# Optimization experiments

Measured on AMD Instinct MI355X. Metric: run time of the kernel, lower is better.

## Reference

```python
import jax, jax.numpy as jnp
import numpy as np

N_NODES = 50000


def gcn_conv(x, row, col, W, b, n_nodes):
    # x: [N, Cin], row/col: [E+N] (self-loops already appended)
    x = x @ W  # [N, Cout]
    deg = jax.ops.segment_sum(jnp.ones(col.shape, x.dtype), col, num_segments=n_nodes)
    dinv = jnp.where(deg > 0, jax.lax.rsqrt(deg), 0.0)
    norm = dinv[row] * dinv[col]  # [E+N]
    msgs = x[row] * norm[:, None]  # gather + scale, [E+N, Cout]
    out = jax.ops.segment_sum(msgs, col, num_segments=n_nodes)
    return out + b


def setup_inputs() -> dict:
    key = jax.random.key(0)
    ks = jax.random.split(key, 5)
    n, e = N_NODES, 640000
    d_in, d_h, d_out = 128, 128, 64
    x = jax.random.normal(ks[0], (n, d_in), dtype=jnp.float32)
    edge_index = jax.random.randint(ks[1], (2, e), 0, n, dtype=jnp.int64)
    s1 = 1.0 / np.sqrt(d_in)
    s2 = 1.0 / np.sqrt(d_h)
    W1 = jax.random.normal(ks[2], (d_in, d_h), dtype=jnp.float32) * s1
    W2 = jax.random.normal(ks[3], (d_h, d_h), dtype=jnp.float32) * s2
    Wl = jax.random.normal(ks[4], (d_h, d_out), dtype=jnp.float32) * s2
    return {
        "x": x, "edge_index": edge_index,
        "W1": W1, "b1": jnp.zeros((d_h,), jnp.float32),
        "W2": W2, "b2": jnp.zeros((d_h,), jnp.float32),
        "Wl": Wl, "bl": jnp.zeros((d_out,), jnp.float32),
    }


def reference(x, edge_index, W1, b1, W2, b2, Wl, bl):
    n = x.shape[0]
    loops = jnp.arange(n, dtype=edge_index.dtype)
    row = jnp.concatenate([edge_index[0], loops])  # add self-loops (PyG GCNConv)
    col = jnp.concatenate([edge_index[1], loops])
    h = jax.nn.relu(gcn_conv(x, row, col, W1, b1, n))  # dropout is identity in eval
    h = jax.nn.relu(gcn_conv(h, row, col, W2, b2, n))
    return h @ Wl + bl
```

## Files before the change

### kernel.cpp

```cpp
#include <hip/hip_runtime.h>

#define NN 50000
#define NE 640000
#define RB ((NN + 255) / 256)

struct __align__(8) edge_t { int r; float w; };

__global__ void k_detect(const unsigned* __restrict__ w, int* __restrict__ flag) {
    __shared__ int found;
    if (threadIdx.x == 0) found = 0;
    __syncthreads();
    int j = threadIdx.x * 2499;
    if (w[2 * j + 1] != 0u) atomicAdd(&found, 1);
    __syncthreads();
    if (threadIdx.x == 0) *flag = (found == 0) ? 1 : 0;
}

__device__ __forceinline__ int edge_at(const void* p, long long i, int m64) {
    if (m64) return (int)((const long long*)p)[i];
    return ((const int*)p)[i];
}

__global__ void k_count(const void* __restrict__ e, const int* __restrict__ flag,
                        int* __restrict__ deg) {
    int i = blockIdx.x * 256 + threadIdx.x;
    if (i >= NE) return;
    int m = *flag;
    int c = edge_at(e, (long long)NE + i, m);
    if ((unsigned)c < (unsigned)NN) atomicAdd(&deg[c], 1);
}

__global__ __launch_bounds__(256) void k_reduce(const int* __restrict__ deg,
                                                int* __restrict__ bsum) {
    __shared__ int s[256];
    int i = blockIdx.x * 256 + threadIdx.x;
    s[threadIdx.x] = (i < NN) ? deg[i] : 0;
    __syncthreads();
    for (int d = 128; d > 0; d >>= 1) {
        if (threadIdx.x < d) s[threadIdx.x] += s[threadIdx.x + d];
        __syncthreads();
    }
    if (threadIdx.x == 0) bsum[blockIdx.x] = s[0];
}

__global__ __launch_bounds__(256) void k_apply(const int* __restrict__ deg,
                                               const int* __restrict__ bsum,
                                               int* __restrict__ offs,
                                               int* __restrict__ cursor,
                                               float* __restrict__ dinv) {
    __shared__ int s[256];
    __shared__ int base_s;
    int t = threadIdx.x;
    int v = (t < RB && t < blockIdx.x) ? bsum[t] : 0;
    s[t] = v;
    __syncthreads();
    for (int d = 128; d > 0; d >>= 1) {
        if (t < d) s[t] += s[t + d];
        __syncthreads();
    }
    if (t == 0) base_s = s[0];
    __syncthreads();
    int base = base_s;
    __syncthreads();
    int i = blockIdx.x * 256 + t;
    int dg = (i < NN) ? deg[i] : 0;
    s[t] = dg;
    __syncthreads();
    for (int d = 1; d < 256; d <<= 1) {
        int u = (t >= d) ? s[t - d] : 0;
        __syncthreads();
        s[t] += u;
        __syncthreads();
    }
    if (i < NN) {
        int excl = base + s[t] - dg;
        offs[i] = excl;
        cursor[i] = excl;
        dinv[i] = rsqrtf((float)(dg + 1));
        if (i == NN - 1) offs[NN] = excl + dg;
    }
}

__global__ void k_scatter(const void* __restrict__ e, const int* __restrict__ flag,
                          int* __restrict__ cursor, edge_t* __restrict__ ew,
                          const float* __restrict__ dinv) {
    int i = blockIdx.x * 256 + threadIdx.x;
    if (i >= NE) return;
    int m = *flag;
    int c = edge_at(e, (long long)NE + i, m);
    if ((unsigned)c >= (unsigned)NN) return;
    int r = edge_at(e, (long long)i, m);
    r = min(max(r, 0), NN - 1);
    int p = atomicAdd(&cursor[c], 1);
    edge_t t2; t2.r = r; t2.w = dinv[r];
    ew[p] = t2;
}

__global__ __launch_bounds__(256) void k_gemm128(const float* __restrict__ A,
                                                 const float* __restrict__ W,
                                                 float* __restrict__ T) {
    __shared__ float Ws[64 * 128];
    int t = threadIdx.x;
    int rg = t >> 4, cg = t & 15;
    int row0 = blockIdx.x * 32 + rg * 2;
    const float4* a0 = (const float4*)(A + (long long)min(row0 + 0, NN - 1) * 128);
    const float4* a1 = (const float4*)(A + (long long)min(row0 + 1, NN - 1) * 128);
    float acc[2][8];
#pragma unroll
    for (int i = 0; i < 2; i++)
#pragma unroll
        for (int j = 0; j < 8; j++) acc[i][j] = 0.f;
#pragma unroll
    for (int h = 0; h < 2; h++) {
        __syncthreads();
#pragma unroll
        for (int i = 0; i < 8; i++)
            ((float4*)Ws)[t + 256 * i] = ((const float4*)(W + h * 64 * 128))[t + 256 * i];
        __syncthreads();
#pragma unroll 4
        for (int k4 = 0; k4 < 16; k4++) {
            float4 av0 = a0[h * 16 + k4];
            float4 av1 = a1[h * 16 + k4];
#pragma unroll
            for (int kk = 0; kk < 4; kk++) {
                float4 w0 = *(const float4*)&Ws[(k4 * 4 + kk) * 128 + cg * 4];
                float4 w1 = *(const float4*)&Ws[(k4 * 4 + kk) * 128 + cg * 4 + 64];
                float x0 = (kk == 0) ? av0.x : (kk == 1) ? av0.y : (kk == 2) ? av0.z : av0.w;
                float x1 = (kk == 0) ? av1.x : (kk == 1) ? av1.y : (kk == 2) ? av1.z : av1.w;
                acc[0][0] += x0 * w0.x; acc[0][1] += x0 * w0.y;
                acc[0][2] += x0 * w0.z; acc[0][3] += x0 * w0.w;
                acc[0][4] += x0 * w1.x; acc[0][5] += x0 * w1.y;
                acc[0][6] += x0 * w1.z; acc[0][7] += x0 * w1.w;
                acc[1][0] += x1 * w0.x; acc[1][1] += x1 * w0.y;
                acc[1][2] += x1 * w0.z; acc[1][3] += x1 * w0.w;
                acc[1][4] += x1 * w1.x; acc[1][5] += x1 * w1.y;
                acc[1][6] += x1 * w1.z; acc[1][7] += x1 * w1.w;
            }
        }
    }
#pragma unroll
    for (int i = 0; i < 2; i++) {
        int row = row0 + i;
        if (row < NN) {
            float4 v0 = {acc[i][0], acc[i][1], acc[i][2], acc[i][3]};
            float4 v1 = {acc[i][4], acc[i][5], acc[i][6], acc[i][7]};
            *(float4*)&T[(long long)row * 128 + cg * 4] = v0;
            *(float4*)&T[(long long)row * 128 + cg * 4 + 64] = v1;
        }
    }
}

__global__ __launch_bounds__(256) void k_gemm64(const float* __restrict__ A,
                                                const float* __restrict__ W,
                                                const float* __restrict__ b,
                                                float* __restrict__ T) {
    __shared__ float Ws[128 * 64];
    int t = threadIdx.x;
#pragma unroll
    for (int i = 0; i < 8; i++)
        ((float4*)Ws)[t + 256 * i] = ((const float4*)W)[t + 256 * i];
    __syncthreads();
    int rg = t >> 4, cg = t & 15;
    int row0 = blockIdx.x * 32 + rg * 2;
    const float4* a0 = (const float4*)(A + (long long)min(row0 + 0, NN - 1) * 128);
    const float4* a1 = (const float4*)(A + (long long)min(row0 + 1, NN - 1) * 128);
    float acc[2][4];
#pragma unroll
    for (int i = 0; i < 2; i++)
#pragma unroll
        for (int j = 0; j < 4; j++) acc[i][j] = 0.f;
#pragma unroll 4
    for (int k4 = 0; k4 < 32; k4++) {
        float4 av0 = a0[k4];
        float4 av1 = a1[k4];
#pragma unroll
        for (int kk = 0; kk < 4; kk++) {
            float4 w = *(const float4*)&Ws[(k4 * 4 + kk) * 64 + cg * 4];
            float x0 = (kk == 0) ? av0.x : (kk == 1) ? av0.y : (kk == 2) ? av0.z : av0.w;
            float x1 = (kk == 0) ? av1.x : (kk == 1) ? av1.y : (kk == 2) ? av1.z : av1.w;
            acc[0][0] += x0 * w.x; acc[0][1] += x0 * w.y;
            acc[0][2] += x0 * w.z; acc[0][3] += x0 * w.w;
            acc[1][0] += x1 * w.x; acc[1][1] += x1 * w.y;
            acc[1][2] += x1 * w.z; acc[1][3] += x1 * w.w;
        }
    }
    float4 bb = ((const float4*)b)[cg];
#pragma unroll
    for (int i = 0; i < 2; i++) {
        int row = row0 + i;
        if (row < NN) {
            float4 v = {acc[i][0] + bb.x, acc[i][1] + bb.y,
                        acc[i][2] + bb.z, acc[i][3] + bb.w};
            *(float4*)&T[(long long)row * 64 + cg * 4] = v;
        }
    }
}

__global__ __launch_bounds__(256) void k_agg(const float* __restrict__ X,
                                             const int* __restrict__ offs,
                                             const edge_t* __restrict__ ew,
                                             const float* __restrict__ dinv,
                                             const float* __restrict__ b,
                                             float* __restrict__ H) {
    int t = threadIdx.x;
    int node = blockIdx.x * 4 + (t >> 6);
    if (node >= NN) return;
    int lane = t & 63;
    int half = lane >> 5;
    int l32 = lane & 31;
    const float4* X4 = (const float4*)X;
    float dc = dinv[node];
    float4 acc = {0.f, 0.f, 0.f, 0.f};
    if (half == 0) {
        float4 s = X4[(long long)node * 32 + l32];
        acc.x = dc * s.x; acc.y = dc * s.y; acc.z = dc * s.z; acc.w = dc * s.w;
    }
    int e0 = offs[node], e1 = offs[node + 1];
    int n = e1 - e0;
    const edge_t* ep = ew + e0;
    int i = half;
    for (; i + 6 < n; i += 8) {
        edge_t m0 = ep[i], m1 = ep[i + 2], m2 = ep[i + 4], m3 = ep[i + 6];
        float4 v0 = X4[(long long)m0.r * 32 + l32];
        float4 v1 = X4[(long long)m1.r * 32 + l32];
        float4 v2 = X4[(long long)m2.r * 32 + l32];
        float4 v3 = X4[(long long)m3.r * 32 + l32];
        acc.x += m0.w * v0.x + m1.w * v1.x + m2.w * v2.x + m3.w * v3.x;
        acc.y += m0.w * v0.y + m1.w * v1.y + m2.w * v2.y + m3.w * v3.y;
        acc.z += m0.w * v0.z + m1.w * v1.z + m2.w * v2.z + m3.w * v3.z;
        acc.w += m0.w * v0.w + m1.w * v1.w + m2.w * v2.w + m3.w * v3.w;
    }
    for (; i < n; i += 2) {
        edge_t m = ep[i];
        float4 v = X4[(long long)m.r * 32 + l32];
        acc.x += m.w * v.x; acc.y += m.w * v.y;
        acc.z += m.w * v.z; acc.w += m.w * v.w;
    }
    float4 oth;
    oth.x = __shfl_xor(acc.x, 32);
    oth.y = __shfl_xor(acc.y, 32);
    oth.z = __shfl_xor(acc.z, 32);
    oth.w = __shfl_xor(acc.w, 32);
    float4 bb = ((const float4*)b)[l32];
    float4 o;
    o.x = fmaxf(dc * (acc.x + oth.x) + bb.x, 0.f);
    o.y = fmaxf(dc * (acc.y + oth.y) + bb.y, 0.f);
    o.z = fmaxf(dc * (acc.z + oth.z) + bb.z, 0.f);
    o.w = fmaxf(dc * (acc.w + oth.w) + bb.w, 0.f);
    if (half == 0)
        ((float4*)H)[(long long)node * 32 + l32] = o;
}

extern "C" void kernel_launch(void* const* d_in, const int* in_sizes, int n_in,
                              void* d_out, int out_size, void* d_ws, size_t ws_size,
                              hipStream_t stream) {
    const float* x  = (const float*)d_in[0];
    const void*  ei = d_in[1];
    const float* W1 = (const float*)d_in[2];
    const float* b1 = (const float*)d_in[3];
    const float* W2 = (const float*)d_in[4];
    const float* b2 = (const float*)d_in[5];
    const float* Wl = (const float*)d_in[6];
    const float* bl = (const float*)d_in[7];
    float* out = (float*)d_out;

    char* ws = (char*)d_ws;
    size_t off = 0;
    auto alloc = [&](size_t bytes) {
        void* p = ws + off;
        off += (bytes + 255) & ~(size_t)255;
        return p;
    };
    float*  t0     = (float*)alloc((size_t)NN * 128 * 4);
    float*  t1     = (float*)alloc((size_t)NN * 128 * 4);
    int*    deg    = (int*)alloc((size_t)NN * 4);
    int*    offs   = (int*)alloc((size_t)(NN + 1) * 4);
    int*    cursor = (int*)alloc((size_t)NN * 4);
    edge_t* ewbuf  = (edge_t*)alloc((size_t)NE * 8);
    float*  dinv   = (float*)alloc((size_t)NN * 4);
    int*    bsum   = (int*)alloc((size_t)RB * 4);
    int*    flag   = (int*)alloc(256);

    hipMemsetAsync(deg, 0, (size_t)NN * 4, stream);
    k_detect<<<1, 256, 0, stream>>>((const unsigned*)ei, flag);
    k_count<<<(NE + 255) / 256, 256, 0, stream>>>(ei, flag, deg);
    k_reduce<<<RB, 256, 0, stream>>>(deg, bsum);
    k_apply<<<RB, 256, 0, stream>>>(deg, bsum, offs, cursor, dinv);
    k_scatter<<<(NE + 255) / 256, 256, 0, stream>>>(ei, flag, cursor, ewbuf, dinv);

    int gb32 = (NN + 31) / 32;
    k_gemm128<<<gb32, 256, 0, stream>>>(x, W1, t0);
    k_agg<<<(NN + 3) / 4, 256, 0, stream>>>(t0, offs, ewbuf, dinv, b1, t1);
    k_gemm128<<<gb32, 256, 0, stream>>>(t1, W2, t0);
    k_agg<<<(NN + 3) / 4, 256, 0, stream>>>(t0, offs, ewbuf, dinv, b2, t1);
    k_gemm64<<<gb32, 256, 0, stream>>>(t1, Wl, bl, out);
}
```

Before: 329.5 us.

## Store transformed features in fp16 for aggregation and inline index-width detection

The GEMM outputs feeding the neighbor aggregation are now stored as fp16, and the aggregation kernel converts them back to fp32 after loading. This halves the bytes moved by the random-access gather, which dominates aggregation cost. Separately, the single-block width-detection kernel is removed and its check is folded into each block of the count and scatter kernels, saving a launch at the cost of a small redundant read per block. The fp16 storage adds rounding error to the hidden features relative to the fp32 reference.

New measurement: 308.0 us. 1.07x faster.

```diff
diff --git a/kernel.cpp b/kernel.cpp
--- a/kernel.cpp
+++ b/kernel.cpp
@@ -1,4 +1,5 @@
 #include <hip/hip_runtime.h>
+#include <hip/hip_fp16.h>
 
 #define NN 50000
 #define NE 640000
@@ -6,26 +7,25 @@
 
 struct __align__(8) edge_t { int r; float w; };
 
-__global__ void k_detect(const unsigned* __restrict__ w, int* __restrict__ flag) {
-    __shared__ int found;
-    if (threadIdx.x == 0) found = 0;
-    __syncthreads();
-    int j = threadIdx.x * 2499;
-    if (w[2 * j + 1] != 0u) atomicAdd(&found, 1);
-    __syncthreads();
-    if (threadIdx.x == 0) *flag = (found == 0) ? 1 : 0;
-}
-
 __device__ __forceinline__ int edge_at(const void* p, long long i, int m64) {
     if (m64) return (int)((const long long*)p)[i];
     return ((const int*)p)[i];
 }
 
-__global__ void k_count(const void* __restrict__ e, const int* __restrict__ flag,
-                        int* __restrict__ deg) {
+__device__ __forceinline__ int detect_m64(const unsigned* w, int tid) {
+    __shared__ int found;
+    if (tid == 0) found = 0;
+    __syncthreads();
+    if (tid < 256 && w[2 * tid + 1] != 0u) atomicAdd(&found, 1);
+    __syncthreads();
+    return (found == 0) ? 1 : 0;
+}
+
+__global__ __launch_bounds__(256) void k_count(const void* __restrict__ e,
+                                               int* __restrict__ deg) {
+    int m = detect_m64((const unsigned*)e, threadIdx.x);
     int i = blockIdx.x * 256 + threadIdx.x;
     if (i >= NE) return;
-    int m = *flag;
     int c = edge_at(e, (long long)NE + i, m);
     if ((unsigned)c < (unsigned)NN) atomicAdd(&deg[c], 1);
 }
@@ -81,12 +81,13 @@
     }
 }
 
-__global__ void k_scatter(const void* __restrict__ e, const int* __restrict__ flag,
-                          int* __restrict__ cursor, edge_t* __restrict__ ew,
-                          const float* __restrict__ dinv) {
+__global__ __launch_bounds__(256) void k_scatter(const void* __restrict__ e,
+                                                 int* __restrict__ cursor,
+                                                 edge_t* __restrict__ ew,
+                                                 const float* __restrict__ dinv) {
+    int m = detect_m64((const unsigned*)e, threadIdx.x);
     int i = blockIdx.x * 256 + threadIdx.x;
     if (i >= NE) return;
-    int m = *flag;
     int c = edge_at(e, (long long)NE + i, m);
     if ((unsigned)c >= (unsigned)NN) return;
     int r = edge_at(e, (long long)i, m);
@@ -96,9 +97,9 @@
     ew[p] = t2;
 }
 
-__global__ __launch_bounds__(256) void k_gemm128(const float* __restrict__ A,
-                                                 const float* __restrict__ W,
-                                                 float* __restrict__ T) {
+__global__ __launch_bounds__(256) void k_gemm128h(const float* __restrict__ A,
+                                                  const float* __restrict__ W,
+                                                  __half* __restrict__ Th) {
     __shared__ float Ws[64 * 128];
     int t = threadIdx.x;
     int rg = t >> 4, cg = t & 15;
@@ -142,10 +143,14 @@
     for (int i = 0; i < 2; i++) {
         int row = row0 + i;
         if (row < NN) {
-            float4 v0 = {acc[i][0], acc[i][1], acc[i][2], acc[i][3]};
-            float4 v1 = {acc[i][4], acc[i][5], acc[i][6], acc[i][7]};
-            *(float4*)&T[(long long)row * 128 + cg * 4] = v0;
-            *(float4*)&T[(long long)row * 128 + cg * 4 + 64] = v1;
+            __half2 p0 = __floats2half2_rn(acc[i][0], acc[i][1]);
+            __half2 p1 = __floats2half2_rn(acc[i][2], acc[i][3]);
+            __half2 p2 = __floats2half2_rn(acc[i][4], acc[i][5]);
+            __half2 p3 = __floats2half2_rn(acc[i][6], acc[i][7]);
+            uint2 u0; u0.x = *(unsigned*)&p0; u0.y = *(unsigned*)&p1;
+            uint2 u1; u1.x = *(unsigned*)&p2; u1.y = *(unsigned*)&p3;
+            *(uint2*)(Th + (long long)row * 128 + cg * 4) = u0;
+            *(uint2*)(Th + (long long)row * 128 + cg * 4 + 64) = u1;
         }
     }
 }
@@ -196,23 +201,32 @@
     }
 }
 
-__global__ __launch_bounds__(256) void k_agg(const float* __restrict__ X,
-                                             const int* __restrict__ offs,
-                                             const edge_t* __restrict__ ew,
-                                             const float* __restrict__ dinv,
-                                             const float* __restrict__ b,
-                                             float* __restrict__ H) {
+__device__ __forceinline__ float4 h4_to_f4(uint2 u) {
+    __half2 h0 = *reinterpret_cast<const __half2*>(&u.x);
+    __half2 h1 = *reinterpret_cast<const __half2*>(&u.y);
+    float2 f0 = __half22float2(h0);
+    float2 f1 = __half22float2(h1);
+    float4 r; r.x = f0.x; r.y = f0.y; r.z = f1.x; r.w = f1.y;
+    return r;
+}
+
+__global__ __launch_bounds__(256) void k_agg_h(const __half* __restrict__ X,
+                                               const int* __restrict__ offs,
+                                               const edge_t* __restrict__ ew,
+                                               const float* __restrict__ dinv,
+                                               const float* __restrict__ b,
+                                               float* __restrict__ H) {
     int t = threadIdx.x;
     int node = blockIdx.x * 4 + (t >> 6);
     if (node >= NN) return;
     int lane = t & 63;
     int half = lane >> 5;
     int l32 = lane & 31;
-    const float4* X4 = (const float4*)X;
+    const uint2* X2 = (const uint2*)X;
     float dc = dinv[node];
     float4 acc = {0.f, 0.f, 0.f, 0.f};
     if (half == 0) {
-        float4 s = X4[(long long)node * 32 + l32];
+        float4 s = h4_to_f4(X2[(long long)node * 32 + l32]);
         acc.x = dc * s.x; acc.y = dc * s.y; acc.z = dc * s.z; acc.w = dc * s.w;
     }
     int e0 = offs[node], e1 = offs[node + 1];
@@ -221,10 +235,12 @@
     int i = half;
     for (; i + 6 < n; i += 8) {
         edge_t m0 = ep[i], m1 = ep[i + 2], m2 = ep[i + 4], m3 = ep[i + 6];
-        float4 v0 = X4[(long long)m0.r * 32 + l32];
-        float4 v1 = X4[(long long)m1.r * 32 + l32];
-        float4 v2 = X4[(long long)m2.r * 32 + l32];
-        float4 v3 = X4[(long long)m3.r * 32 + l32];
+        uint2 u0 = X2[(long long)m0.r * 32 + l32];
+        uint2 u1 = X2[(long long)m1.r * 32 + l32];
+        uint2 u2 = X2[(long long)m2.r * 32 + l32];
+        uint2 u3 = X2[(long long)m3.r * 32 + l32];
+        float4 v0 = h4_to_f4(u0), v1 = h4_to_f4(u1);
+        float4 v2 = h4_to_f4(u2), v3 = h4_to_f4(u3);
         acc.x += m0.w * v0.x + m1.w * v1.x + m2.w * v2.x + m3.w * v3.x;
         acc.y += m0.w * v0.y + m1.w * v1.y + m2.w * v2.y + m3.w * v3.y;
         acc.z += m0.w * v0.z + m1.w * v1.z + m2.w * v2.z + m3.w * v3.z;
@@ -232,7 +248,7 @@
     }
     for (; i < n; i += 2) {
         edge_t m = ep[i];
-        float4 v = X4[(long long)m.r * 32 + l32];
+        float4 v = h4_to_f4(X2[(long long)m.r * 32 + l32]);
         acc.x += m.w * v.x; acc.y += m.w * v.y;
         acc.z += m.w * v.z; acc.w += m.w * v.w;
     }
@@ -271,7 +287,7 @@
         off += (bytes + 255) & ~(size_t)255;
         return p;
     };
-    float*  t0     = (float*)alloc((size_t)NN * 128 * 4);
+    __half* t0h    = (__half*)alloc((size_t)NN * 128 * 2);
     float*  t1     = (float*)alloc((size_t)NN * 128 * 4);
     int*    deg    = (int*)alloc((size_t)NN * 4);
     int*    offs   = (int*)alloc((size_t)(NN + 1) * 4);
@@ -279,19 +295,17 @@
     edge_t* ewbuf  = (edge_t*)alloc((size_t)NE * 8);
     float*  dinv   = (float*)alloc((size_t)NN * 4);
     int*    bsum   = (int*)alloc((size_t)RB * 4);
-    int*    flag   = (int*)alloc(256);
 
     hipMemsetAsync(deg, 0, (size_t)NN * 4, stream);
-    k_detect<<<1, 256, 0, stream>>>((const unsigned*)ei, flag);
-    k_count<<<(NE + 255) / 256, 256, 0, stream>>>(ei, flag, deg);
+    k_count<<<(NE + 255) / 256, 256, 0, stream>>>(ei, deg);
     k_reduce<<<RB, 256, 0, stream>>>(deg, bsum);
     k_apply<<<RB, 256, 0, stream>>>(deg, bsum, offs, cursor, dinv);
-    k_scatter<<<(NE + 255) / 256, 256, 0, stream>>>(ei, flag, cursor, ewbuf, dinv);
+    k_scatter<<<(NE + 255) / 256, 256, 0, stream>>>(ei, cursor, ewbuf, dinv);
 
     int gb32 = (NN + 31) / 32;
-    k_gemm128<<<gb32, 256, 0, stream>>>(x, W1, t0);
-    k_agg<<<(NN + 3) / 4, 256, 0, stream>>>(t0, offs, ewbuf, dinv, b1, t1);
-    k_gemm128<<<gb32, 256, 0, stream>>>(t1, W2, t0);
-    k_agg<<<(NN + 3) / 4, 256, 0, stream>>>(t0, offs, ewbuf, dinv, b2, t1);
+    k_gemm128h<<<gb32, 256, 0, stream>>>(x, W1, t0h);
+    k_agg_h<<<(NN + 3) / 4, 256, 0, stream>>>(t0h, offs, ewbuf, dinv, b1, t1);
+    k_gemm128h<<<gb32, 256, 0, stream>>>(t1, W2, t0h);
+    k_agg_h<<<(NN + 3) / 4, 256, 0, stream>>>(t0h, offs, ewbuf, dinv, b2, t1);
     k_gemm64<<<gb32, 256, 0, stream>>>(t1, Wl, bl, out);
 }
```
